# Performance work log

Hardware: AMD Instinct MI355X
Metric: run time of the kernel (lower is better)

## Reference

```python
import jax, jax.numpy as jnp
import numpy as np

jax.config.update("jax_enable_x64", True)  # original numpy code runs in float64

B, T, D = 8, 1600, 64
WINDOW, TAK_DIM, TAK_TAU = 50, 3, 1
N_RADII, N_BINS, N_FEAT = 20, 20, 8
N = WINDOW - (TAK_DIM - 1) * TAK_TAU          # 48 points per Takens cloud
L_CAP = N * (N - 1) // 2                      # hard upper bound on beta_1
_OFF = np.where(~np.eye(N, dtype=bool))      # static off-diagonal indices
EIG_TOL = 1e-6


def setup_inputs():
    key = jax.random.key(0)
    k1, k2, k3 = jax.random.split(key, 3)
    latent_seq = jax.random.normal(k1, (B, T, D), dtype=jnp.float32)
    W = jax.random.normal(k2, (N_FEAT, N_FEAT), dtype=jnp.float32) / np.sqrt(N_FEAT)
    b = jax.random.normal(k3, (N_FEAT,), dtype=jnp.float32) * 0.01
    return {"latent_seq": latent_seq, "W": W, "b": b}


def _pairwise(X):
    sq = jnp.sum(X * X, axis=1)
    D2 = sq[:, None] + sq[None, :] - 2.0 * (X @ X.T)
    return jnp.sqrt(jnp.maximum(D2, 0.0))


def _prim_deaths(Dm):
    # MST edge weights == H0 death times of single-linkage (Kruskal) for generic weights
    BIG = jnp.asarray(1e30, Dm.dtype)
    def step(carry, _):
        in_tree, mind = carry
        cand = jnp.where(in_tree, BIG, mind)
        j = jnp.argmin(cand)
        w = cand[j]
        in_tree = in_tree.at[j].set(True)
        mind = jnp.minimum(mind, Dm[j])
        return (in_tree, mind), w
    in0 = jnp.zeros((N,), bool).at[0].set(True)
    _, deaths = jax.lax.scan(step, (in0, Dm[0]), None, length=N - 1)
    return deaths


def _entropy(lifetimes, valid):
    lt = jnp.where(valid & (lifetimes > 0), lifetimes, 0.0)
    s = jnp.sum(lt)
    p = lt / jnp.where(s > 0, s, 1.0)
    ent = -jnp.sum(jnp.where(p > 0, p * jnp.log(p), 0.0))
    return jnp.where(s > 0, ent, 0.0)


def _landscape_integral(births, deaths, valid):
    # k=1 persistence landscape on N_BINS grid, summarized by its mean
    has = jnp.any(valid)
    t0 = jnp.where(has, jnp.min(jnp.where(valid, births, jnp.inf)), 0.0)
    t1 = jnp.where(has, jnp.max(jnp.where(valid, deaths, -jnp.inf)), 1.0)
    t = jnp.linspace(t0, t1, N_BINS)
    tent = jnp.minimum(t[:, None] - births[None, :], deaths[None, :] - t[:, None])
    tent = jnp.where(valid[None, :], tent, -jnp.inf)
    lam = jnp.maximum(jnp.max(tent, axis=1), 0.0)
    return jnp.where(has, jnp.mean(lam), 0.0)


def _window_features(cloud):
    Dm = _pairwise(cloud)                       # (N, N)
    vals = Dm[_OFF]                             # all positive off-diagonal distances
    radii = jnp.percentile(vals, jnp.linspace(10.0, 90.0, N_RADII))
    r_med = jnp.median(vals)

    # ---- H0 (exact): single-linkage deaths via vectorized Prim MST
    deaths0 = _prim_deaths(Dm)                  # (N-1,)
    valid0 = jnp.ones(deaths0.shape, bool)
    beta0 = jnp.sum(deaths0 > r_med).astype(Dm.dtype)
    ent0 = _entropy(deaths0, valid0)
    maxp0 = jnp.max(deaths0)
    land0 = _landscape_integral(jnp.zeros_like(deaths0), deaths0, valid0)

    # ---- H1 (spectral proxy): Laplacian eigendecomposition per filtration radius
    offmask = ~jnp.eye(N, dtype=bool)
    A = (Dm[None, :, :] <= radii[:, None, None]) & offmask   # (R, N, N)
    Af = A.astype(jnp.float64)
    deg = Af.sum(-1)                             # (R, N)
    ii = jnp.arange(N)
    Lap = (-Af).at[:, ii, ii].set(deg)
    eig = jnp.linalg.eigvalsh(Lap)               # (R, N), ascending
    comps = jnp.sum(eig < EIG_TOL, axis=1)
    edges = jnp.sum(A, axis=(1, 2)) // 2
    beta1 = jnp.maximum(0, edges - N + comps)    # (R,) int, prev_beta1 starts at 0

    # LIFO birth/death pair tracking == per-level run extraction of (beta1 >= l)
    lev = jnp.arange(1, L_CAP + 1)
    Alev = beta1[None, :] >= lev[:, None]                      # (L_CAP, R)
    prev = jnp.concatenate([jnp.zeros((L_CAP, 1), bool), Alev[:, :-1]], axis=1)
    starts = Alev & ~prev
    ends = (~Alev) & prev                                      # finite deaths only
    step_idx = jnp.arange(N_RADII)
    last_start = jax.lax.cummax(jnp.where(starts, step_idx, -1), axis=1)
    births1 = radii[jnp.clip(last_start, 0)]                   # (L_CAP, R)
    deathr1 = jnp.broadcast_to(radii[None, :], (L_CAP, N_RADII))
    life1 = deathr1 - births1
    beta1_med = jnp.sum(ends & (births1 <= r_med) & (r_med < deathr1)).astype(Dm.dtype)
    ent1 = _entropy(life1.ravel(), ends.ravel())
    maxp1 = jnp.max(jnp.where(ends, life1, 0.0))
    land1 = _landscape_integral(births1.ravel(), deathr1.ravel(), ends.ravel())

    return jnp.stack([beta0, beta1_med, ent0, ent1, maxp0, maxp1, land0, land1]).astype(jnp.float32)


def _topo_features(latent_seq):
    series = jnp.linalg.norm(latent_seq, axis=-1)   # (B, T) scalar series per step
    nw = T // WINDOW
    wins = series[:, : nw * WINDOW].reshape(B * nw, WINDOW)
    tak = np.arange(N)[:, None] + np.arange(TAK_DIM)[None, :] * TAK_TAU
    clouds = wins[:, tak]                           # (B*nw, N, TAK_DIM) Takens embedding
    feats = jax.vmap(_window_features)(clouds)      # (B*nw, 8)
    return feats.reshape(B, nw, N_FEAT)


def reference(latent_seq, W, b):
    feats = _topo_features(latent_seq)              # torch version is @no_grad
    return feats @ W.T + b                          # feature_proj: Linear(8, 8)
```

## Files before the change

kernel.cpp:

```cpp
#include <hip/hip_runtime.h>
#include <math.h>

#define T_LEN 1600
#define D_DIM 64
#define WIN   50
#define NPT   48
#define NPAIR 1128
#define VPL   18
#define K_MED 563

template <typename F>
__device__ __forceinline__ int dpp_red63(int v, F op) {
    int t;
    t = __builtin_amdgcn_update_dpp(v, v, 0xb1, 0xf, 0xf, false); v = op(v, t);
    t = __builtin_amdgcn_update_dpp(v, v, 0x4e, 0xf, 0xf, false); v = op(v, t);
    t = __builtin_amdgcn_update_dpp(v, v, 0x114, 0xf, 0xe, false); v = op(v, t);
    t = __builtin_amdgcn_update_dpp(v, v, 0x118, 0xf, 0xc, false); v = op(v, t);
    t = __builtin_amdgcn_update_dpp(v, v, 0x142, 0xa, 0xf, false); v = op(v, t);
    t = __builtin_amdgcn_update_dpp(v, v, 0x143, 0xc, 0xf, false); v = op(v, t);
    return v;
}
__device__ __forceinline__ float wave_fmin_bc(float v) {
    int r = dpp_red63(__float_as_int(v), [](int a, int b) {
        return __float_as_int(fminf(__int_as_float(a), __int_as_float(b))); });
    return __int_as_float(__builtin_amdgcn_readlane(r, 63));
}
__device__ __forceinline__ float wave_fmax_bc(float v) {
    int r = dpp_red63(__float_as_int(v), [](int a, int b) {
        return __float_as_int(fmaxf(__int_as_float(a), __int_as_float(b))); });
    return __int_as_float(__builtin_amdgcn_readlane(r, 63));
}
__device__ __forceinline__ float wave_fadd_bc(float v) {
    int r = dpp_red63(__float_as_int(v), [](int a, int b) {
        return __float_as_int(__fadd_rn(__int_as_float(a), __int_as_float(b))); });
    return __int_as_float(__builtin_amdgcn_readlane(r, 63));
}
__device__ __forceinline__ unsigned wave_umin_bc(unsigned v) {
    int r = dpp_red63((int)v, [](int a, int b) {
        unsigned ua = (unsigned)a, ub = (unsigned)b;
        return (int)(ua < ub ? ua : ub); });
    return (unsigned)__builtin_amdgcn_readlane(r, 63);
}

__global__ __launch_bounds__(256)
void topo_feats_kernel(const float* __restrict__ latent,
                       const float* __restrict__ W,
                       const float* __restrict__ bvec,
                       float* __restrict__ out)
{
    __shared__ float s_series[WIN];
    __shared__ float s_sq[NPT];
    __shared__ float s_D[NPT * NPT];
    __shared__ float s_med;

    const int w    = blockIdx.x;
    const int bb   = w >> 5;
    const int kk   = w & 31;
    const int tid  = threadIdx.x;
    const int wv   = tid >> 6;
    const int lane = tid & 63;

    float pb = 0.0f, pw0 = 0.0f, pw2 = 0.0f, pw4 = 0.0f, pw6 = 0.0f;
    if (wv == 0 && lane < 8) {
        pb  = bvec[lane];
        pw0 = W[lane * 8 + 0];
        pw2 = W[lane * 8 + 2];
        pw4 = W[lane * 8 + 4];
        pw6 = W[lane * 8 + 6];
    }

    if (wv == 0) {
        float x0 = 0.0f;
        if (lane < WIN) {
            const float4* p4 = (const float4*)(latent +
                ((size_t)bb * T_LEN + (size_t)kk * WIN + lane) * D_DIM);
            float r[8];
#pragma unroll
            for (int q = 0; q < 8; ++q) r[q] = 0.0f;
#pragma unroll
            for (int i = 0; i < 16; i += 2) {
                float4 a = p4[i], b = p4[i + 1];
                r[0] = __fadd_rn(r[0], __fmul_rn(a.x, a.x));
                r[1] = __fadd_rn(r[1], __fmul_rn(a.y, a.y));
                r[2] = __fadd_rn(r[2], __fmul_rn(a.z, a.z));
                r[3] = __fadd_rn(r[3], __fmul_rn(a.w, a.w));
                r[4] = __fadd_rn(r[4], __fmul_rn(b.x, b.x));
                r[5] = __fadd_rn(r[5], __fmul_rn(b.y, b.y));
                r[6] = __fadd_rn(r[6], __fmul_rn(b.z, b.z));
                r[7] = __fadd_rn(r[7], __fmul_rn(b.w, b.w));
            }
            float ss = __fadd_rn(__fadd_rn(__fadd_rn(r[0], r[1]), __fadd_rn(r[2], r[3])),
                                 __fadd_rn(__fadd_rn(r[4], r[5]), __fadd_rn(r[6], r[7])));
            x0 = sqrtf(ss);
        }
        float x1 = __shfl_down(x0, 1);
        float x2 = __shfl_down(x0, 2);
        if (lane < WIN) s_series[lane] = x0;
        if (lane < NPT)
            s_sq[lane] = __fadd_rn(__fadd_rn(__fmul_rn(x0, x0), __fmul_rn(x1, x1)),
                                   __fmul_rn(x2, x2));
    }
    __syncthreads();

    for (int e = tid; e < NPT * NPT; e += 256) {
        int i = e / NPT, j = e - i * NPT;
        float dot = fmaf(s_series[i + 2], s_series[j + 2],
                    fmaf(s_series[i + 1], s_series[j + 1],
                         __fmul_rn(s_series[i], s_series[j])));
        float d2 = __fsub_rn(__fadd_rn(s_sq[i], s_sq[j]), __fmul_rn(2.0f, dot));
        s_D[i * NPT + j] = sqrtf(fmaxf(d2, 0.0f));
    }
    __syncthreads();

    float dreg = 0.0f;

    if (wv == 0) {
        bool  intree = (lane == 0);
        float mind   = (lane < NPT) ? s_D[lane] : 1e30f;
        for (int it = 0; it < NPT - 1; ++it) {
            float cand = (intree || lane >= NPT) ? 1e30f : mind;
            float wmin = wave_fmin_bc(cand);
            if (lane == it) dreg = wmin;
            unsigned long long m = __ballot(cand == wmin);
            int id = __ffsll(m) - 1;
            if (lane == id) intree = true;
            if (lane < NPT) mind = fminf(mind, s_D[id * NPT + lane]);
        }
    } else if (wv == 1) {
        unsigned ub[VPL];
#pragma unroll
        for (int r = 0; r < VPL; ++r) {
            int e = lane + 64 * r;
            unsigned v = 0xFFFFFFFFu;
            if (e < NPAIR) {
                int i = (int)((95.0f - sqrtf((float)(9025 - 8 * e))) * 0.5f);
                i = (i < 0) ? 0 : ((i > NPT - 2) ? NPT - 2 : i);
                int offi = (i * (95 - i)) >> 1;
                int offn = ((i + 1) * (94 - i)) >> 1;
                if (e >= offn)      { ++i; offi = offn; }
                else if (e < offi)  { --i; offi = (i * (95 - i)) >> 1; }
                int j = i + 1 + (e - offi);
                v = __float_as_uint(s_D[i * NPT + j]);
            }
            ub[r] = v;
        }
        unsigned lo = 0;
        for (int bit = 30; bit >= 0; --bit) {
            unsigned probe = lo | (1u << bit);
            int c = 0;
#pragma unroll
            for (int r = 0; r < VPL; ++r)
                c += __popcll(__ballot(ub[r] < probe));
            if (c <= K_MED) lo = probe;
        }
        const unsigned v0 = lo;
        int cle = 0; unsigned mn = 0xFFFFFFFFu;
#pragma unroll
        for (int r = 0; r < VPL; ++r) {
            cle += __popcll(__ballot(ub[r] <= v0));
            if (ub[r] > v0 && ub[r] < mn) mn = ub[r];
        }
        mn = wave_umin_bc(mn);
        unsigned v1 = (cle >= K_MED + 2) ? v0 : mn;
        if (lane == 0)
            s_med = __fadd_rn(__fmul_rn(0.5f, __uint_as_float(v0)),
                              __fmul_rn(0.5f, __uint_as_float(v1)));
    }
    __syncthreads();

    if (wv == 0) {
        const float rmed = s_med;
        const bool  isd  = (lane < NPT - 1);
        const float d    = isd ? dreg : 0.0f;

        float beta0 = (float)__popcll(__ballot(isd && (d > rmed)));
        float mx    = wave_fmax_bc(isd ? d : -INFINITY);

        float sv = (isd && d > 0.0f) ? d : 0.0f;
        float ss = wave_fadd_bc(sv);

        float p    = sv / ss;
        float term = (p > 0.0f) ? -p * logf(p) : 0.0f;
        float ent  = wave_fadd_bc(term);

        float step = mx / 19.0f;
        float t    = step * (float)lane;
        float lam  = (lane < 20) ? fmaxf(fminf(t, mx - t), 0.0f) : 0.0f;
        float land = wave_fadd_bc(lam) * (1.0f / 20.0f);

        if (lane < 8) {
            float o = pb + beta0 * pw0 + ent * pw2 + mx * pw4 + land * pw6;
            out[w * 8 + lane] = o;
        }
    }
}

extern "C" void kernel_launch(void* const* d_in, const int* in_sizes, int n_in,
                              void* d_out, int out_size, void* d_ws, size_t ws_size,
                              hipStream_t stream)
{
    const float* latent = (const float*)d_in[0];
    const float* W      = (const float*)d_in[1];
    const float* bvec   = (const float*)d_in[2];
    float*       out    = (float*)d_out;

    topo_feats_kernel<<<dim3(256), dim3(256), 0, stream>>>(latent, W, bvec, out);

    (void)in_sizes; (void)n_in; (void)out_size; (void)d_ws; (void)ws_size;
}
```

Measured before the change: 18.96 us.

## Pack four windows per block with paired Prim and median waves

Each 512-thread block now handles four windows instead of one. Waves 0-3 run the Prim MST for their window, and waves 4-7 run the median bit-search for the matching window. The pairwise distance matrix for each window is built by two waves. This removes the idle waves of the old 256-thread layout, where only two of four waves did serial work. The cost is fewer blocks (64 instead of 256), so fewer CUs are occupied on a large GPU.

```diff
diff --git a/kernel.cpp b/kernel.cpp
--- a/kernel.cpp
+++ b/kernel.cpp
@@ -8,6 +8,7 @@
 #define NPAIR 1128
 #define VPL   18
 #define K_MED 563
+#define WPB   4
 
 template <typename F>
 __device__ __forceinline__ int dpp_red63(int v, F op) {
@@ -42,26 +43,27 @@
     return (unsigned)__builtin_amdgcn_readlane(r, 63);
 }
 
-__global__ __launch_bounds__(256)
+__global__ __launch_bounds__(512)
 void topo_feats_kernel(const float* __restrict__ latent,
                        const float* __restrict__ W,
                        const float* __restrict__ bvec,
                        float* __restrict__ out)
 {
-    __shared__ float s_series[WIN];
-    __shared__ float s_sq[NPT];
-    __shared__ float s_D[NPT * NPT];
-    __shared__ float s_med;
-
-    const int w    = blockIdx.x;
-    const int bb   = w >> 5;
-    const int kk   = w & 31;
+    __shared__ float s_series[WPB][WIN];
+    __shared__ float s_sq[WPB][NPT];
+    __shared__ float s_D[WPB][NPT * NPT];
+    __shared__ float s_med[WPB];
+
     const int tid  = threadIdx.x;
     const int wv   = tid >> 6;
     const int lane = tid & 63;
+    const int q    = wv & 3;
+    const int w    = blockIdx.x * WPB + q;
+    const int bb   = w >> 5;
+    const int kk   = w & 31;
 
     float pb = 0.0f, pw0 = 0.0f, pw2 = 0.0f, pw4 = 0.0f, pw6 = 0.0f;
-    if (wv == 0 && lane < 8) {
+    if (wv < 4 && lane < 8) {
         pb  = bvec[lane];
         pw0 = W[lane * 8 + 0];
         pw2 = W[lane * 8 + 2];
@@ -69,14 +71,14 @@
         pw6 = W[lane * 8 + 6];
     }
 
-    if (wv == 0) {
+    if (wv < 4) {
         float x0 = 0.0f;
         if (lane < WIN) {
             const float4* p4 = (const float4*)(latent +
                 ((size_t)bb * T_LEN + (size_t)kk * WIN + lane) * D_DIM);
             float r[8];
 #pragma unroll
-            for (int q = 0; q < 8; ++q) r[q] = 0.0f;
+            for (int i = 0; i < 8; ++i) r[i] = 0.0f;
 #pragma unroll
             for (int i = 0; i < 16; i += 2) {
                 float4 a = p4[i], b = p4[i + 1];
@@ -95,28 +97,33 @@
         }
         float x1 = __shfl_down(x0, 1);
         float x2 = __shfl_down(x0, 2);
-        if (lane < WIN) s_series[lane] = x0;
+        if (lane < WIN) s_series[q][lane] = x0;
         if (lane < NPT)
-            s_sq[lane] = __fadd_rn(__fadd_rn(__fmul_rn(x0, x0), __fmul_rn(x1, x1)),
-                                   __fmul_rn(x2, x2));
+            s_sq[q][lane] = __fadd_rn(__fadd_rn(__fmul_rn(x0, x0), __fmul_rn(x1, x1)),
+                                      __fmul_rn(x2, x2));
     }
     __syncthreads();
 
-    for (int e = tid; e < NPT * NPT; e += 256) {
-        int i = e / NPT, j = e - i * NPT;
-        float dot = fmaf(s_series[i + 2], s_series[j + 2],
-                    fmaf(s_series[i + 1], s_series[j + 1],
-                         __fmul_rn(s_series[i], s_series[j])));
-        float d2 = __fsub_rn(__fadd_rn(s_sq[i], s_sq[j]), __fmul_rn(2.0f, dot));
-        s_D[i * NPT + j] = sqrtf(fmaxf(d2, 0.0f));
+    {
+        const int sub = (wv >> 2) & 1;
+#pragma unroll
+        for (int k = 0; k < NPT * NPT / 128; ++k) {
+            int e = lane + 64 * sub + 128 * k;
+            int i = e / NPT, j = e - i * NPT;
+            float dot = fmaf(s_series[q][i + 2], s_series[q][j + 2],
+                        fmaf(s_series[q][i + 1], s_series[q][j + 1],
+                             __fmul_rn(s_series[q][i], s_series[q][j])));
+            float d2 = __fsub_rn(__fadd_rn(s_sq[q][i], s_sq[q][j]), __fmul_rn(2.0f, dot));
+            s_D[q][i * NPT + j] = sqrtf(fmaxf(d2, 0.0f));
+        }
     }
     __syncthreads();
 
     float dreg = 0.0f;
 
-    if (wv == 0) {
+    if (wv < 4) {
         bool  intree = (lane == 0);
-        float mind   = (lane < NPT) ? s_D[lane] : 1e30f;
+        float mind   = (lane < NPT) ? s_D[q][lane] : 1e30f;
         for (int it = 0; it < NPT - 1; ++it) {
             float cand = (intree || lane >= NPT) ? 1e30f : mind;
             float wmin = wave_fmin_bc(cand);
@@ -124,9 +131,9 @@
             unsigned long long m = __ballot(cand == wmin);
             int id = __ffsll(m) - 1;
             if (lane == id) intree = true;
-            if (lane < NPT) mind = fminf(mind, s_D[id * NPT + lane]);
-        }
-    } else if (wv == 1) {
+            if (lane < NPT) mind = fminf(mind, s_D[q][id * NPT + lane]);
+        }
+    } else {
         unsigned ub[VPL];
 #pragma unroll
         for (int r = 0; r < VPL; ++r) {
@@ -140,7 +147,7 @@
                 if (e >= offn)      { ++i; offi = offn; }
                 else if (e < offi)  { --i; offi = (i * (95 - i)) >> 1; }
                 int j = i + 1 + (e - offi);
-                v = __float_as_uint(s_D[i * NPT + j]);
+                v = __float_as_uint(s_D[q][i * NPT + j]);
             }
             ub[r] = v;
         }
@@ -163,13 +170,13 @@
         mn = wave_umin_bc(mn);
         unsigned v1 = (cle >= K_MED + 2) ? v0 : mn;
         if (lane == 0)
-            s_med = __fadd_rn(__fmul_rn(0.5f, __uint_as_float(v0)),
-                              __fmul_rn(0.5f, __uint_as_float(v1)));
+            s_med[q] = __fadd_rn(__fmul_rn(0.5f, __uint_as_float(v0)),
+                                 __fmul_rn(0.5f, __uint_as_float(v1)));
     }
     __syncthreads();
 
-    if (wv == 0) {
-        const float rmed = s_med;
+    if (wv < 4) {
+        const float rmed = s_med[q];
         const bool  isd  = (lane < NPT - 1);
         const float d    = isd ? dreg : 0.0f;
 
@@ -204,7 +211,7 @@
     const float* bvec   = (const float*)d_in[2];
     float*       out    = (float*)d_out;
 
-    topo_feats_kernel<<<dim3(256), dim3(256), 0, stream>>>(latent, W, bvec, out);
+    topo_feats_kernel<<<dim3(256 / WPB), dim3(512), 0, stream>>>(latent, W, bvec, out);
 
     (void)in_sizes; (void)n_in; (void)out_size; (void)d_ws; (void)ws_size;
 }
```

Result: slower. 21.96 us (+15.8%).
